# Kernel optimization log

Hardware: AMD Instinct MI355X
Metric: run time of the kernel (lower is better)

Reference implementation:

```python
import jax, jax.numpy as jnp
import numpy as np

BS, NC, Nc, D_n = 8, 256, 128, 64
ALPHA, HS, HM = 2, 256, 128
GAMMA_MAX = 0.5
EPS = 1e-6


def setup_inputs() -> dict:
    key = jax.random.key(0)
    ks = jax.random.split(key, 12)
    f = jax.random.normal
    return {
        "x": f(ks[0], (BS, NC, D_n), jnp.float32),
        "h": f(ks[1], (BS, NC, Nc, D_n), jnp.float32) * 0.1,
        "W": f(ks[2], (BS, NC, Nc, Nc), jnp.float32) * (Nc ** -0.5),
        "decay": jax.random.uniform(ks[3], (BS, NC, Nc), jnp.float32),
        "hebbian": f(ks[4], (BS, NC, Nc, Nc), jnp.float32) * 0.01,
        "neuron_id": f(ks[5], (NC, Nc, D_n), jnp.float32) * (D_n ** -0.5),
        "state_w1": f(ks[6], (HS, 2 * D_n), jnp.float32) * ((2 * D_n) ** -0.5),
        "state_b1": jnp.zeros((HS,), jnp.float32),
        "state_w2": f(ks[7], (D_n, HS), jnp.float32) * (HS ** -0.5),
        "state_b2": jnp.zeros((D_n,), jnp.float32),
        "msg_w1": f(ks[8], (HM, D_n), jnp.float32) * (D_n ** -0.5),
        "msg_b1": jnp.zeros((HM,), jnp.float32),
        "msg_w2": f(ks[9], (D_n, HM), jnp.float32) * (HM ** -0.5),
        "msg_b2": jnp.zeros((D_n,), jnp.float32),
        "inject_w": f(ks[10], (NC, ALPHA * D_n, D_n), jnp.float32) * (D_n ** -0.5),
        "inject_b": jnp.zeros((NC, ALPHA * D_n), jnp.float32),
        "W_decay_logit": jnp.full((NC, Nc), -3.0, jnp.float32),
        "decay_gamma_logit": jnp.full((NC, Nc), -3.0, jnp.float32),
        "hebbian_decay_logit": jnp.full((NC, Nc), 2.0, jnp.float32),
    }


def _rms_norm(v):
    # F.rms_norm over the last (Nc) axis, no affine weight
    return v * jax.lax.rsqrt(jnp.mean(v * v, axis=-1, keepdims=True) + EPS)


def reference(x, h, W, decay, hebbian, neuron_id,
              state_w1, state_b1, state_w2, state_b2,
              msg_w1, msg_b1, msg_w2, msg_b2,
              inject_w, inject_b,
              W_decay_logit, decay_gamma_logit, hebbian_decay_logit):
    B = x.shape[0]
    # per-cell injection of external input into the first ALPHA neurons
    inj = jnp.einsum('bcd,cad->bca', x, inject_w) + inject_b   # [B,NC,ALPHA*D_n]
    h = h.at[:, :, :ALPHA, :].add(inj.reshape(B, NC, ALPHA, D_n))
    h_id = h + neuron_id                                       # identity embedding broadcast
    # per-neuron message MLP (tanh hidden)
    m = jnp.tanh(jnp.einsum('bcnd,hd->bcnh', h_id, msg_w1) + msg_b1)
    m = jnp.einsum('bcnh,dh->bcnd', m, msg_w2) + msg_b2        # [B,NC,Nc,D_n]
    # Hebbian-weighted adjacency message passing: small per-cell matmul W @ m
    agg = jnp.einsum('bcij,bcjd->bcid', W, m)
    # state update MLP on concat(state, aggregated message)
    s = jnp.tanh(jnp.einsum('bcnd,hd->bcnh',
                            jnp.concatenate([h_id, agg], axis=-1), state_w1) + state_b1)
    dh = jnp.einsum('bcnh,dh->bcnd', s, state_w2) + state_b2
    # gated decay of per-neuron state
    dg = GAMMA_MAX * jax.nn.sigmoid(decay_gamma_logit)         # [NC,Nc]
    decay_new = (1.0 - dg) * decay + dg * jax.nn.sigmoid(jnp.mean(dh, axis=-1))
    h_new = (1.0 - decay_new[..., None]) * h + decay_new[..., None] * jnp.tanh(dh)
    # Hebbian outer-product plasticity
    hg = GAMMA_MAX * jax.nn.sigmoid(hebbian_decay_logit)
    outer = jnp.einsum('bcid,bcjd->bcij', h_new, m) / D_n
    hebbian_new = (1.0 - hg[..., None]) * hebbian + hg[..., None] * outer
    # decayed adjacency update + rms-norm over the incoming-edge axis
    wg = GAMMA_MAX * jax.nn.sigmoid(W_decay_logit)
    W_new = _rms_norm((1.0 - wg[..., None]) * W + wg[..., None] * hebbian_new)
    return (h_new, m, W_new, decay_new, hebbian_new)
```

## Files before the change

kernel.cpp:

```cpp
#include <hip/hip_runtime.h>


#define NCELL 256

typedef __attribute__((ext_vector_type(8))) short bf16x8;
typedef __attribute__((ext_vector_type(4))) float f32x4;

#define MFMA(a, b, c) __builtin_amdgcn_mfma_f32_16x16x32_bf16((a), (b), (c), 0, 0, 0)

__device__ __forceinline__ unsigned short f2bf(float f) {
    unsigned u = __builtin_bit_cast(unsigned, f);
    u = (u + 0x7FFFu + ((u >> 16) & 1u)) >> 16;
    return (unsigned short)u;
}
__device__ __forceinline__ float bf2f(unsigned short b) {
    unsigned u = ((unsigned)b) << 16;
    return __builtin_bit_cast(float, u);
}
__device__ __forceinline__ float sigm(float v) { return 1.0f / (1.0f + __expf(-v)); }

__device__ __forceinline__ int sw64(int row, int col) {
    return row * 64 + ((((col >> 3) ^ row) & 7) << 3) + (col & 7);
}
__device__ __forceinline__ int sw128(int row, int col) {
    return row * 128 + (((col >> 3) ^ (row & 7)) << 3) + (col & 7);
}
__device__ __forceinline__ int sw32(int row, int col) {
    return row * 32 + ((((col >> 3) ^ row) & 3) << 3) + (col & 7);
}

__global__ void cvt_w(const float* __restrict__ a, const float* __restrict__ b,
                      const float* __restrict__ c, const float* __restrict__ d,
                      unsigned short* __restrict__ dst) {
    int i = blockIdx.x * 256 + threadIdx.x;
    float v;
    if (i < 8192) v = a[i];
    else if (i < 16384) v = b[i - 8192];
    else if (i < 49152) v = c[i - 16384];
    else v = d[i - 49152];
    dst[i] = f2bf(v);
}

__global__ __launch_bounds__(256, 2)
void cell_kernel(const float* __restrict__ x, const float* __restrict__ h,
                 const float* __restrict__ W, const float* __restrict__ decay,
                 const float* __restrict__ hebb, const float* __restrict__ nid,
                 const float* __restrict__ sb1, const float* __restrict__ sb2,
                 const float* __restrict__ mb1, const float* __restrict__ mb2,
                 const float* __restrict__ injw, const float* __restrict__ injb,
                 const float* __restrict__ wdl, const float* __restrict__ dgl,
                 const float* __restrict__ hdl,
                 const unsigned short* __restrict__ wbf,
                 float* __restrict__ out) {
    const int cell = blockIdx.x;
    const int c = cell & (NCELL - 1);
    const int tid = threadIdx.x;
    const int wv = tid >> 6;
    const int lane = tid & 63;
    const int lr = lane & 15;
    const int lg = lane >> 4;

    float* out_h  = out;
    float* out_m  = out + 16777216;
    float* out_W  = out + 33554432;
    float* out_d  = out + 67108864;
    float* out_hb = out + 67371008;

    const unsigned short* w1m = wbf;
    const unsigned short* w2m = wbf + 8192;
    const unsigned short* w1s = wbf + 16384;
    const unsigned short* w2s = wbf + 49152;

    __shared__ alignas(16) unsigned char smem[73728];
    unsigned short* hid_s = (unsigned short*)smem;
    unsigned short* m_s   = (unsigned short*)(smem + 16384);
    unsigned short* mT_s  = (unsigned short*)(smem + 32768);
    unsigned short* agg_s = (unsigned short*)(smem + 49152);
    unsigned short* hbuf  = (unsigned short*)(smem + 65536) + wv * 1024;
    float* inj_s = (float*)(smem + 49152);

    if (tid < 128) {
        const float* iwr = injw + (c * 128 + tid) * 64;
        const float* xr = x + cell * 64;
        float acc = injb[c * 128 + tid];
        #pragma unroll
        for (int d4 = 0; d4 < 16; ++d4) {
            float4 a = ((const float4*)iwr)[d4];
            float4 xv = ((const float4*)xr)[d4];
            acc += a.x * xv.x + a.y * xv.y + a.z * xv.z + a.w * xv.w;
        }
        inj_s[tid] = acc;
    }
    __syncthreads();

    {
        const int row = wv * 32 + (lane >> 1);
        const int colbase = (lane & 1) * 32;
        const float* hr = h + (size_t)(cell * 128 + row) * 64;
        const float* nr = nid + (size_t)(c * 128 + row) * 64;
        #pragma unroll
        for (int g = 0; g < 4; ++g) {
            int col = colbase + g * 8;
            float4 a0 = *(const float4*)(hr + col);
            float4 a1 = *(const float4*)(hr + col + 4);
            float4 n0 = *(const float4*)(nr + col);
            float4 n1 = *(const float4*)(nr + col + 4);
            float v[8] = {a0.x, a0.y, a0.z, a0.w, a1.x, a1.y, a1.z, a1.w};
            float nn[8] = {n0.x, n0.y, n0.z, n0.w, n1.x, n1.y, n1.z, n1.w};
            unsigned short us[8];
            #pragma unroll
            for (int j = 0; j < 8; ++j) {
                float hv = v[j];
                if (row < 2) hv += inj_s[row * 64 + col + j];
                hv += nn[j];
                us[j] = f2bf(hv);
            }
            *(bf16x8*)&hid_s[sw64(row, col)] = *(bf16x8*)us;
        }
    }

    bf16x8 aH[2][2];
    #pragma unroll
    for (int rt = 0; rt < 2; ++rt)
        #pragma unroll
        for (int ks = 0; ks < 2; ++ks)
            aH[rt][ks] = *(const bf16x8*)&hid_s[sw64(wv * 32 + rt * 16 + lr, ks * 32 + lg * 8)];

    f32x4 accM[2][4];
    #pragma unroll
    for (int rt = 0; rt < 2; ++rt)
        #pragma unroll
        for (int dt = 0; dt < 4; ++dt)
            accM[rt][dt] = (f32x4){0.f, 0.f, 0.f, 0.f};

    #pragma unroll
    for (int ch = 0; ch < 4; ++ch) {
        f32x4 accH[2][2];
        #pragma unroll
        for (int rt = 0; rt < 2; ++rt)
            #pragma unroll
            for (int ht = 0; ht < 2; ++ht)
                accH[rt][ht] = (f32x4){0.f, 0.f, 0.f, 0.f};
        #pragma unroll
        for (int ks = 0; ks < 2; ++ks)
            #pragma unroll
            for (int ht = 0; ht < 2; ++ht) {
                bf16x8 bw = *(const bf16x8*)&w1m[(ch * 32 + ht * 16 + lr) * 64 + ks * 32 + lg * 8];
                #pragma unroll
                for (int rt = 0; rt < 2; ++rt)
                    accH[rt][ht] = MFMA(aH[rt][ks], bw, accH[rt][ht]);
            }
        #pragma unroll
        for (int rt = 0; rt < 2; ++rt)
            #pragma unroll
            for (int ht = 0; ht < 2; ++ht) {
                float b1v = mb1[ch * 32 + ht * 16 + lr];
                #pragma unroll
                for (int r = 0; r < 4; ++r) {
                    float t = tanhf(accH[rt][ht][r] + b1v);
                    hbuf[sw32(rt * 16 + lg * 4 + r, ht * 16 + lr)] = f2bf(t);
                }
            }
        #pragma unroll
        for (int rt = 0; rt < 2; ++rt) {
            bf16x8 aM = *(const bf16x8*)&hbuf[sw32(rt * 16 + lr, lg * 8)];
            #pragma unroll
            for (int dt = 0; dt < 4; ++dt) {
                bf16x8 bw = *(const bf16x8*)&w2m[(dt * 16 + lr) * 128 + ch * 32 + lg * 8];
                accM[rt][dt] = MFMA(aM, bw, accM[rt][dt]);
            }
        }
    }
    #pragma unroll
    for (int rt = 0; rt < 2; ++rt)
        #pragma unroll
        for (int dt = 0; dt < 4; ++dt) {
            float b2v = mb2[dt * 16 + lr];
            #pragma unroll
            for (int r = 0; r < 4; ++r) {
                float mv = accM[rt][dt][r] + b2v;
                int n = wv * 32 + rt * 16 + lg * 4 + r;
                int dcol = dt * 16 + lr;
                out_m[(size_t)(cell * 128 + n) * 64 + dcol] = mv;
                unsigned short mb = f2bf(mv);
                m_s[sw64(n, dcol)] = mb;
                mT_s[sw128(dcol, n)] = mb;
            }
        }
    __syncthreads();

    f32x4 accA[2][4];
    #pragma unroll
    for (int rt = 0; rt < 2; ++rt)
        #pragma unroll
        for (int dt = 0; dt < 4; ++dt)
            accA[rt][dt] = (f32x4){0.f, 0.f, 0.f, 0.f};
    {
        const float* Wbase = W + (size_t)cell * 128 * 128;
        #pragma unroll
        for (int ks = 0; ks < 4; ++ks)
            #pragma unroll
            for (int rt = 0; rt < 2; ++rt) {
                const float* wr = Wbase + (wv * 32 + rt * 16 + lr) * 128 + ks * 32 + lg * 8;
                float4 wa = *(const float4*)wr;
                float4 wb = *(const float4*)(wr + 4);
                unsigned short uw[8] = {f2bf(wa.x), f2bf(wa.y), f2bf(wa.z), f2bf(wa.w),
                                        f2bf(wb.x), f2bf(wb.y), f2bf(wb.z), f2bf(wb.w)};
                bf16x8 aW = *(bf16x8*)uw;
                #pragma unroll
                for (int dt = 0; dt < 4; ++dt) {
                    bf16x8 bm = *(const bf16x8*)&mT_s[sw128(dt * 16 + lr, ks * 32 + lg * 8)];
                    accA[rt][dt] = MFMA(aW, bm, accA[rt][dt]);
                }
            }
    }
    #pragma unroll
    for (int rt = 0; rt < 2; ++rt)
        #pragma unroll
        for (int dt = 0; dt < 4; ++dt)
            #pragma unroll
            for (int r = 0; r < 4; ++r)
                agg_s[sw64(wv * 32 + rt * 16 + lg * 4 + r, dt * 16 + lr)] = f2bf(accA[rt][dt][r]);

    bf16x8 aG[2][2];
    #pragma unroll
    for (int rt = 0; rt < 2; ++rt)
        #pragma unroll
        for (int ks = 0; ks < 2; ++ks)
            aG[rt][ks] = *(const bf16x8*)&agg_s[sw64(wv * 32 + rt * 16 + lr, ks * 32 + lg * 8)];

    f32x4 accD[2][4];
    #pragma unroll
    for (int rt = 0; rt < 2; ++rt)
        #pragma unroll
        for (int dt = 0; dt < 4; ++dt)
            accD[rt][dt] = (f32x4){0.f, 0.f, 0.f, 0.f};

    #pragma unroll
    for (int ch = 0; ch < 8; ++ch) {
        f32x4 accS[2][2];
        #pragma unroll
        for (int rt = 0; rt < 2; ++rt)
            #pragma unroll
            for (int ht = 0; ht < 2; ++ht)
                accS[rt][ht] = (f32x4){0.f, 0.f, 0.f, 0.f};
        #pragma unroll
        for (int ks = 0; ks < 4; ++ks)
            #pragma unroll
            for (int ht = 0; ht < 2; ++ht) {
                bf16x8 bw = *(const bf16x8*)&w1s[(ch * 32 + ht * 16 + lr) * 128 + ks * 32 + lg * 8];
                #pragma unroll
                for (int rt = 0; rt < 2; ++rt) {
                    bf16x8 af = (ks < 2) ? aH[rt][ks] : aG[rt][ks - 2];
                    accS[rt][ht] = MFMA(af, bw, accS[rt][ht]);
                }
            }
        #pragma unroll
        for (int rt = 0; rt < 2; ++rt)
            #pragma unroll
            for (int ht = 0; ht < 2; ++ht) {
                float bv = sb1[ch * 32 + ht * 16 + lr];
                #pragma unroll
                for (int r = 0; r < 4; ++r) {
                    float t = tanhf(accS[rt][ht][r] + bv);
                    hbuf[sw32(rt * 16 + lg * 4 + r, ht * 16 + lr)] = f2bf(t);
                }
            }
        #pragma unroll
        for (int rt = 0; rt < 2; ++rt) {
            bf16x8 aS = *(const bf16x8*)&hbuf[sw32(rt * 16 + lr, lg * 8)];
            #pragma unroll
            for (int dt = 0; dt < 4; ++dt) {
                bf16x8 bw = *(const bf16x8*)&w2s[(dt * 16 + lr) * 256 + ch * 32 + lg * 8];
                accD[rt][dt] = MFMA(aS, bw, accD[rt][dt]);
            }
        }
    }

    float dnew_r[2][4];
    #pragma unroll
    for (int rt = 0; rt < 2; ++rt)
        #pragma unroll
        for (int r = 0; r < 4; ++r) {
            float s = 0.f;
            #pragma unroll
            for (int dt = 0; dt < 4; ++dt) {
                accD[rt][dt][r] += sb2[dt * 16 + lr];
                s += accD[rt][dt][r];
            }
            s += __shfl_xor(s, 1);
            s += __shfl_xor(s, 2);
            s += __shfl_xor(s, 4);
            s += __shfl_xor(s, 8);
            int row = wv * 32 + rt * 16 + lg * 4 + r;
            float mean = s * (1.0f / 64.0f);
            float dg = 0.5f * sigm(dgl[c * 128 + row]);
            float dn = (1.0f - dg) * decay[cell * 128 + row] + dg * sigm(mean);
            if (lr == 0) out_d[cell * 128 + row] = dn;
            dnew_r[rt][r] = dn;
        }
    #pragma unroll
    for (int rt = 0; rt < 2; ++rt)
        #pragma unroll
        for (int r = 0; r < 4; ++r) {
            int row = wv * 32 + rt * 16 + lg * 4 + r;
            float dn = dnew_r[rt][r];
            #pragma unroll
            for (int dt = 0; dt < 4; ++dt) {
                int col = dt * 16 + lr;
                float hpost = bf2f(hid_s[sw64(row, col)]) - nid[(size_t)(c * 128 + row) * 64 + col];
                float hn = (1.0f - dn) * hpost + dn * tanhf(accD[rt][dt][r]);
                out_h[(size_t)(cell * 128 + row) * 64 + col] = hn;
                hid_s[sw64(row, col)] = f2bf(hn);
            }
        }

    bf16x8 aO[2][2];
    #pragma unroll
    for (int rt = 0; rt < 2; ++rt)
        #pragma unroll
        for (int ks = 0; ks < 2; ++ks)
            aO[rt][ks] = *(const bf16x8*)&hid_s[sw64(wv * 32 + rt * 16 + lr, ks * 32 + lg * 8)];

    f32x4 accO[2][8];
    #pragma unroll
    for (int rt = 0; rt < 2; ++rt)
        #pragma unroll
        for (int jt = 0; jt < 8; ++jt)
            accO[rt][jt] = (f32x4){0.f, 0.f, 0.f, 0.f};
    #pragma unroll
    for (int jt = 0; jt < 8; ++jt)
        #pragma unroll
        for (int ks = 0; ks < 2; ++ks) {
            bf16x8 bm = *(const bf16x8*)&m_s[sw64(jt * 16 + lr, ks * 32 + lg * 8)];
            #pragma unroll
            for (int rt = 0; rt < 2; ++rt)
                accO[rt][jt] = MFMA(aO[rt][ks], bm, accO[rt][jt]);
        }

    #pragma unroll
    for (int rt = 0; rt < 2; ++rt)
        #pragma unroll
        for (int r = 0; r < 4; ++r) {
            int i = wv * 32 + rt * 16 + lg * 4 + r;
            float hg = 0.5f * sigm(hdl[c * 128 + i]);
            float wg = 0.5f * sigm(wdl[c * 128 + i]);
            const float* hbr = hebb + (size_t)(cell * 128 + i) * 128;
            const float* Wr = W + (size_t)(cell * 128 + i) * 128;
            float* ohb = out_hb + (size_t)(cell * 128 + i) * 128;
            float wpre[8];
            float ss = 0.f;
            #pragma unroll
            for (int jt = 0; jt < 8; ++jt) {
                int j = jt * 16 + lr;
                float o = accO[rt][jt][r] * (1.0f / 64.0f);
                float hbn = (1.0f - hg) * hbr[j] + hg * o;
                ohb[j] = hbn;
                float wp = (1.0f - wg) * Wr[j] + wg * hbn;
                wpre[jt] = wp;
                ss += wp * wp;
            }
            ss += __shfl_xor(ss, 1);
            ss += __shfl_xor(ss, 2);
            ss += __shfl_xor(ss, 4);
            ss += __shfl_xor(ss, 8);
            float scale = rsqrtf(ss * (1.0f / 128.0f) + 1e-6f);
            float* oW = out_W + (size_t)(cell * 128 + i) * 128;
            #pragma unroll
            for (int jt = 0; jt < 8; ++jt)
                oW[jt * 16 + lr] = wpre[jt] * scale;
        }
}

extern "C" void kernel_launch(void* const* d_in, const int* in_sizes, int n_in,
                              void* d_out, int out_size, void* d_ws, size_t ws_size,
                              hipStream_t stream) {
    const float* x    = (const float*)d_in[0];
    const float* h    = (const float*)d_in[1];
    const float* W    = (const float*)d_in[2];
    const float* dec  = (const float*)d_in[3];
    const float* hebb = (const float*)d_in[4];
    const float* nid  = (const float*)d_in[5];
    const float* sw1  = (const float*)d_in[6];
    const float* sb1  = (const float*)d_in[7];
    const float* sw2  = (const float*)d_in[8];
    const float* sb2  = (const float*)d_in[9];
    const float* mw1  = (const float*)d_in[10];
    const float* mb1  = (const float*)d_in[11];
    const float* mw2  = (const float*)d_in[12];
    const float* mb2  = (const float*)d_in[13];
    const float* injw = (const float*)d_in[14];
    const float* injb = (const float*)d_in[15];
    const float* wdl  = (const float*)d_in[16];
    const float* dgl  = (const float*)d_in[17];
    const float* hdl  = (const float*)d_in[18];

    unsigned short* wbf = (unsigned short*)d_ws;

    cvt_w<<<256, 256, 0, stream>>>(mw1, mw2, sw1, sw2, wbf);
    cell_kernel<<<2048, 256, 0, stream>>>(x, h, W, dec, hebb, nid, sb1, sb2, mb1, mb2,
                                          injw, injb, wdl, dgl, hdl, wbf, (float*)d_out);
}
```

Measured before the change: 342.1 us.

## Shrink LDS for higher occupancy, fast tanh/sigmoid, prefetch W into registers

Replaces tanhf and the sigmoid division with exp plus hardware reciprocal approximations. Removes the hid_s and agg_s LDS buffers by building the first MFMA operand directly in registers and reusing one staging buffer, cutting shared memory so launch bounds can request 3 blocks per CU. W tiles are loaded into registers at kernel start to overlap their latency with the message MLP. The pre-update state is recomputed from global h plus the injection term instead of subtracting nid from the bf16 copy. The cost is more register pressure and a risk of spills under the tighter register cap.

```diff
diff --git a/kernel.cpp b/kernel.cpp
--- a/kernel.cpp
+++ b/kernel.cpp
@@ -17,7 +17,12 @@
     unsigned u = ((unsigned)b) << 16;
     return __builtin_bit_cast(float, u);
 }
-__device__ __forceinline__ float sigm(float v) { return 1.0f / (1.0f + __expf(-v)); }
+__device__ __forceinline__ float frcp(float x) { return __builtin_amdgcn_rcpf(x); }
+__device__ __forceinline__ float sigm(float v) { return frcp(1.0f + __expf(-v)); }
+__device__ __forceinline__ float ftanh(float x) {
+    float e = __expf(2.0f * x);
+    return 1.0f - 2.0f * frcp(e + 1.0f);
+}
 
 __device__ __forceinline__ int sw64(int row, int col) {
     return row * 64 + ((((col >> 3) ^ row) & 7) << 3) + (col & 7);
@@ -41,7 +46,7 @@
     dst[i] = f2bf(v);
 }
 
-__global__ __launch_bounds__(256, 2)
+__global__ __launch_bounds__(256, 3)
 void cell_kernel(const float* __restrict__ x, const float* __restrict__ h,
                  const float* __restrict__ W, const float* __restrict__ decay,
                  const float* __restrict__ hebb, const float* __restrict__ nid,
@@ -71,13 +76,25 @@
     const unsigned short* w1s = wbf + 16384;
     const unsigned short* w2s = wbf + 49152;
 
-    __shared__ alignas(16) unsigned char smem[73728];
-    unsigned short* hid_s = (unsigned short*)smem;
-    unsigned short* m_s   = (unsigned short*)(smem + 16384);
-    unsigned short* mT_s  = (unsigned short*)(smem + 32768);
-    unsigned short* agg_s = (unsigned short*)(smem + 49152);
-    unsigned short* hbuf  = (unsigned short*)(smem + 65536) + wv * 1024;
+    __shared__ alignas(16) unsigned char smem[49664];
+    unsigned short* m_s  = (unsigned short*)smem;
+    unsigned short* mT_s = (unsigned short*)(smem + 16384);
+    unsigned short* st_s = (unsigned short*)(smem + 32768);
     float* inj_s = (float*)(smem + 49152);
+    unsigned short* hbuf = st_s + wv * 2048;
+
+    float4 wpa[4][2][2];
+    {
+        const float* Wbase = W + (size_t)cell * 16384;
+        #pragma unroll
+        for (int ks = 0; ks < 4; ++ks)
+            #pragma unroll
+            for (int rt = 0; rt < 2; ++rt) {
+                const float* wr = Wbase + (wv * 32 + rt * 16 + lr) * 128 + ks * 32 + lg * 8;
+                wpa[ks][rt][0] = *(const float4*)wr;
+                wpa[ks][rt][1] = *(const float4*)(wr + 4);
+            }
+    }
 
     if (tid < 128) {
         const float* iwr = injw + (c * 128 + tid) * 64;
@@ -93,38 +110,30 @@
     }
     __syncthreads();
 
-    {
-        const int row = wv * 32 + (lane >> 1);
-        const int colbase = (lane & 1) * 32;
-        const float* hr = h + (size_t)(cell * 128 + row) * 64;
-        const float* nr = nid + (size_t)(c * 128 + row) * 64;
-        #pragma unroll
-        for (int g = 0; g < 4; ++g) {
-            int col = colbase + g * 8;
-            float4 a0 = *(const float4*)(hr + col);
-            float4 a1 = *(const float4*)(hr + col + 4);
-            float4 n0 = *(const float4*)(nr + col);
-            float4 n1 = *(const float4*)(nr + col + 4);
+    bf16x8 aH[2][2];
+    #pragma unroll
+    for (int rt = 0; rt < 2; ++rt)
+        #pragma unroll
+        for (int ks = 0; ks < 2; ++ks) {
+            const int row = wv * 32 + rt * 16 + lr;
+            const int col = ks * 32 + lg * 8;
+            const float* hr = h + (size_t)(cell * 128 + row) * 64 + col;
+            const float* nr = nid + (size_t)(c * 128 + row) * 64 + col;
+            float4 a0 = *(const float4*)hr;
+            float4 a1 = *(const float4*)(hr + 4);
+            float4 n0 = *(const float4*)nr;
+            float4 n1 = *(const float4*)(nr + 4);
             float v[8] = {a0.x, a0.y, a0.z, a0.w, a1.x, a1.y, a1.z, a1.w};
             float nn[8] = {n0.x, n0.y, n0.z, n0.w, n1.x, n1.y, n1.z, n1.w};
             unsigned short us[8];
             #pragma unroll
             for (int j = 0; j < 8; ++j) {
-                float hv = v[j];
+                float hv = v[j] + nn[j];
                 if (row < 2) hv += inj_s[row * 64 + col + j];
-                hv += nn[j];
                 us[j] = f2bf(hv);
             }
-            *(bf16x8*)&hid_s[sw64(row, col)] = *(bf16x8*)us;
-        }
-    }
-
-    bf16x8 aH[2][2];
-    #pragma unroll
-    for (int rt = 0; rt < 2; ++rt)
-        #pragma unroll
-        for (int ks = 0; ks < 2; ++ks)
-            aH[rt][ks] = *(const bf16x8*)&hid_s[sw64(wv * 32 + rt * 16 + lr, ks * 32 + lg * 8)];
+            aH[rt][ks] = *(bf16x8*)us;
+        }
 
     f32x4 accM[2][4];
     #pragma unroll
@@ -157,7 +166,7 @@
                 float b1v = mb1[ch * 32 + ht * 16 + lr];
                 #pragma unroll
                 for (int r = 0; r < 4; ++r) {
-                    float t = tanhf(accH[rt][ht][r] + b1v);
+                    float t = ftanh(accH[rt][ht][r] + b1v);
                     hbuf[sw32(rt * 16 + lg * 4 + r, ht * 16 + lr)] = f2bf(t);
                 }
             }
@@ -195,39 +204,35 @@
         #pragma unroll
         for (int dt = 0; dt < 4; ++dt)
             accA[rt][dt] = (f32x4){0.f, 0.f, 0.f, 0.f};
-    {
-        const float* Wbase = W + (size_t)cell * 128 * 128;
-        #pragma unroll
-        for (int ks = 0; ks < 4; ++ks)
-            #pragma unroll
-            for (int rt = 0; rt < 2; ++rt) {
-                const float* wr = Wbase + (wv * 32 + rt * 16 + lr) * 128 + ks * 32 + lg * 8;
-                float4 wa = *(const float4*)wr;
-                float4 wb = *(const float4*)(wr + 4);
-                unsigned short uw[8] = {f2bf(wa.x), f2bf(wa.y), f2bf(wa.z), f2bf(wa.w),
-                                        f2bf(wb.x), f2bf(wb.y), f2bf(wb.z), f2bf(wb.w)};
-                bf16x8 aW = *(bf16x8*)uw;
-                #pragma unroll
-                for (int dt = 0; dt < 4; ++dt) {
-                    bf16x8 bm = *(const bf16x8*)&mT_s[sw128(dt * 16 + lr, ks * 32 + lg * 8)];
-                    accA[rt][dt] = MFMA(aW, bm, accA[rt][dt]);
-                }
-            }
-    }
+    #pragma unroll
+    for (int ks = 0; ks < 4; ++ks)
+        #pragma unroll
+        for (int rt = 0; rt < 2; ++rt) {
+            float4 wa = wpa[ks][rt][0];
+            float4 wb = wpa[ks][rt][1];
+            unsigned short uw[8] = {f2bf(wa.x), f2bf(wa.y), f2bf(wa.z), f2bf(wa.w),
+                                    f2bf(wb.x), f2bf(wb.y), f2bf(wb.z), f2bf(wb.w)};
+            bf16x8 aW = *(bf16x8*)uw;
+            #pragma unroll
+            for (int dt = 0; dt < 4; ++dt) {
+                bf16x8 bm = *(const bf16x8*)&mT_s[sw128(dt * 16 + lr, ks * 32 + lg * 8)];
+                accA[rt][dt] = MFMA(aW, bm, accA[rt][dt]);
+            }
+        }
     #pragma unroll
     for (int rt = 0; rt < 2; ++rt)
         #pragma unroll
         for (int dt = 0; dt < 4; ++dt)
             #pragma unroll
             for (int r = 0; r < 4; ++r)
-                agg_s[sw64(wv * 32 + rt * 16 + lg * 4 + r, dt * 16 + lr)] = f2bf(accA[rt][dt][r]);
+                st_s[sw64(wv * 32 + rt * 16 + lg * 4 + r, dt * 16 + lr)] = f2bf(accA[rt][dt][r]);
 
     bf16x8 aG[2][2];
     #pragma unroll
     for (int rt = 0; rt < 2; ++rt)
         #pragma unroll
         for (int ks = 0; ks < 2; ++ks)
-            aG[rt][ks] = *(const bf16x8*)&agg_s[sw64(wv * 32 + rt * 16 + lr, ks * 32 + lg * 8)];
+            aG[rt][ks] = *(const bf16x8*)&st_s[sw64(wv * 32 + rt * 16 + lr, ks * 32 + lg * 8)];
 
     f32x4 accD[2][4];
     #pragma unroll
@@ -262,7 +267,7 @@
                 float bv = sb1[ch * 32 + ht * 16 + lr];
                 #pragma unroll
                 for (int r = 0; r < 4; ++r) {
-                    float t = tanhf(accS[rt][ht][r] + bv);
+                    float t = ftanh(accS[rt][ht][r] + bv);
                     hbuf[sw32(rt * 16 + lg * 4 + r, ht * 16 + lr)] = f2bf(t);
                 }
             }
@@ -305,13 +310,15 @@
         for (int r = 0; r < 4; ++r) {
             int row = wv * 32 + rt * 16 + lg * 4 + r;
             float dn = dnew_r[rt][r];
+            const float* hr = h + (size_t)(cell * 128 + row) * 64;
             #pragma unroll
             for (int dt = 0; dt < 4; ++dt) {
                 int col = dt * 16 + lr;
-                float hpost = bf2f(hid_s[sw64(row, col)]) - nid[(size_t)(c * 128 + row) * 64 + col];
-                float hn = (1.0f - dn) * hpost + dn * tanhf(accD[rt][dt][r]);
+                float hpost = hr[col];
+                if (row < 2) hpost += inj_s[row * 64 + col];
+                float hn = (1.0f - dn) * hpost + dn * ftanh(accD[rt][dt][r]);
                 out_h[(size_t)(cell * 128 + row) * 64 + col] = hn;
-                hid_s[sw64(row, col)] = f2bf(hn);
+                st_s[sw64(row, col)] = f2bf(hn);
             }
         }
 
@@ -320,7 +327,7 @@
     for (int rt = 0; rt < 2; ++rt)
         #pragma unroll
         for (int ks = 0; ks < 2; ++ks)
-            aO[rt][ks] = *(const bf16x8*)&hid_s[sw64(wv * 32 + rt * 16 + lr, ks * 32 + lg * 8)];
+            aO[rt][ks] = *(const bf16x8*)&st_s[sw64(wv * 32 + rt * 16 + lr, ks * 32 + lg * 8)];
 
     f32x4 accO[2][8];
     #pragma unroll
```

Result: slower. 355.1 us (+3.8%).
